# Kernel optimization log

Hardware: AMD Instinct MI355X
Metric: run time of the kernel (lower is better)

Reference implementation:

```python
import jax, jax.numpy as jnp
import numpy as np

B, L1, NUM_C, DIM_S, SIZE_M = 64, 199, 1000, 64, 50


def setup_inputs() -> dict:
    key = jax.random.key(0)
    ks = jax.random.split(key, 16)
    inp = {
        "cseqs": jax.random.randint(ks[0], (B, L1), 0, NUM_C),
        "rseqs": jax.random.randint(ks[1], (B, L1), 0, 2),
        "shft_cseqs": jax.random.randint(ks[2], (B, L1), 0, NUM_C),
        "shft_rseqs": jax.random.randint(ks[3], (B, L1), 0, 2),
        # learned parameters (linear weights stored as [in, out])
        "kemb": jax.random.normal(ks[4], (NUM_C, DIM_S)) * 0.05,
        "vemb": jax.random.normal(ks[5], (2 * NUM_C, DIM_S)) * 0.05,
        "Mk": jax.random.normal(ks[6], (SIZE_M, DIM_S)) * (2.0 / DIM_S) ** 0.5,
        "Mv0": jax.random.normal(ks[7], (SIZE_M, DIM_S)) * (2.0 / DIM_S) ** 0.5,
        "Wf": jax.random.normal(ks[8], (2 * DIM_S, DIM_S)) * 0.05,
        "bf": jnp.zeros((DIM_S,)),
        "We": jax.random.normal(ks[9], (DIM_S, DIM_S)) * 0.05,
        "be": jnp.zeros((DIM_S,)),
        "Wa": jax.random.normal(ks[10], (DIM_S, DIM_S)) * 0.05,
        "ba": jnp.zeros((DIM_S,)),
        "Wp": jax.random.normal(ks[11], (DIM_S, 1)) * 0.05,
        "bp": jnp.zeros((1,)),
    }
    return inp


def reference(cseqs, rseqs, shft_cseqs, shft_rseqs,
              kemb, vemb, Mk, Mv0, Wf, bf, We, be, Wa, ba, Wp, bp):
    # reconstruct full-length sequences: [B, L] with L = L1 + 1
    q = jnp.concatenate([cseqs[:, :1], shft_cseqs], axis=-1)
    r = jnp.concatenate([rseqs[:, :1], shft_rseqs], axis=-1)
    x = q + NUM_C * r

    k = kemb[q]                                  # [B, L, D]
    v = vemb[x]                                  # [B, L, D]

    w = jax.nn.softmax(k @ Mk.T, axis=-1)        # [B, L, M] correlation weights
    e = jax.nn.sigmoid(v @ We + be)              # [B, L, D] erase
    a = jnp.tanh(v @ Wa + ba)                    # [B, L, D] add

    def step(Mvt, inp):
        et, at, wt = inp                         # [B,D], [B,D], [B,M]
        Mv_prev = Mvt                            # memory BEFORE this update (used for read)
        Mvt = Mvt * (1.0 - wt[:, :, None] * et[:, None, :]) + wt[:, :, None] * at[:, None, :]
        return Mvt, Mv_prev

    Mv_init = jnp.broadcast_to(Mv0[None], (B, SIZE_M, DIM_S))
    _, Mv_prev = jax.lax.scan(
        step, Mv_init,
        (e.transpose(1, 0, 2), a.transpose(1, 0, 2), w.transpose(1, 0, 2)))
    Mv_prev = Mv_prev.transpose(1, 0, 2, 3)      # [B, L, M, D]

    read = jnp.einsum('blm,blmd->bld', w, Mv_prev)   # weighted read
    info = jnp.concatenate([read, k], axis=-1)       # [B, L, 2D]
    f = jnp.tanh(info @ Wf + bf)                     # dropout is identity in eval
    p = jax.nn.sigmoid((f @ Wp + bp).squeeze(-1))    # [B, L]
    return p
```

## Files before the change

### kernel.cpp

```cpp
#include <hip/hip_runtime.h>
#include <math.h>

#define B    64
#define L1   199
#define L    200
#define NC   1000
#define D    64
#define M    50
#define NCH  10
#define MC   5
#define TCC  50

__global__ __launch_bounds__(64) void phase0(
    const float* __restrict__ kemb, const float* __restrict__ vemb,
    const float* __restrict__ Mk,
    const float* __restrict__ We, const float* __restrict__ be,
    const float* __restrict__ Wa, const float* __restrict__ ba,
    const float* __restrict__ Wf,
    float* __restrict__ wtab, float* __restrict__ etab,
    float* __restrict__ atab, float* __restrict__ ktab)
{
    __shared__ __align__(16) float lrow[4 * D];
    const int lane = threadIdx.x;
    const int bid  = blockIdx.x;

    if (bid < 250) {
        const int r0 = bid * 4;
        #pragma unroll
        for (int i = 0; i < 4; ++i)
            lrow[i * D + lane] = kemb[(size_t)(r0 + i) * D + lane];
        __syncthreads();

        float Mk_r[D];
        {
            const int mrow = (lane < M) ? lane : (M - 1);
            #pragma unroll
            for (int d = 0; d < D; d += 4) {
                const float4 t4 = *(const float4*)(Mk + mrow * D + d);
                Mk_r[d] = t4.x; Mk_r[d+1] = t4.y; Mk_r[d+2] = t4.z; Mk_r[d+3] = t4.w;
            }
        }
        #pragma unroll
        for (int i = 0; i < 4; ++i) {
            float c0 = 0.f, c1 = 0.f;
            #pragma unroll
            for (int d = 0; d < D; d += 4) {
                const float4 kb = *(const float4*)&lrow[i * D + d];
                c0 = fmaf(Mk_r[d],     kb.x, c0);
                c1 = fmaf(Mk_r[d + 1], kb.y, c1);
                c0 = fmaf(Mk_r[d + 2], kb.z, c0);
                c1 = fmaf(Mk_r[d + 3], kb.w, c1);
            }
            const float logit = (lane < M) ? (c0 + c1) : -INFINITY;
            float mx = logit;
            #pragma unroll
            for (int off = 32; off; off >>= 1) mx = fmaxf(mx, __shfl_xor(mx, off, 64));
            const float ex = expf(logit - mx);
            float sm = ex;
            #pragma unroll
            for (int off = 32; off; off >>= 1) sm += __shfl_xor(sm, off, 64);
            if (lane < M) wtab[(size_t)(r0 + i) * M + lane] = ex / sm;
        }
    } else if (bid < 1250) {
        const bool is_e = (bid < 750);
        const int  r0   = (is_e ? (bid - 250) : (bid - 750)) * 4;
        #pragma unroll
        for (int i = 0; i < 4; ++i)
            lrow[i * D + lane] = vemb[(size_t)(r0 + i) * D + lane];
        __syncthreads();

        const float* __restrict__ W   = is_e ? We : Wa;
        float*       __restrict__ dst = is_e ? etab : atab;
        float Wc[D];
        #pragma unroll
        for (int din = 0; din < D; ++din) Wc[din] = W[din * D + lane];
        const float br = is_e ? be[lane] : ba[lane];

        #pragma unroll
        for (int i = 0; i < 4; ++i) {
            float c0 = 0.f, c1 = 0.f;
            #pragma unroll
            for (int d = 0; d < D; d += 4) {
                const float4 vb = *(const float4*)&lrow[i * D + d];
                c0 = fmaf(Wc[d],     vb.x, c0);
                c1 = fmaf(Wc[d + 1], vb.y, c1);
                c0 = fmaf(Wc[d + 2], vb.z, c0);
                c1 = fmaf(Wc[d + 3], vb.w, c1);
            }
            const float acc = c0 + c1;
            const float r = is_e ? (1.f / (1.f + expf(-(acc + br))))
                                 : tanhf(acc + br);
            dst[(size_t)(r0 + i) * D + lane] = r;
        }
    } else {
        const int r0 = (bid - 1250) * 4;
        #pragma unroll
        for (int i = 0; i < 4; ++i)
            lrow[i * D + lane] = kemb[(size_t)(r0 + i) * D + lane];
        __syncthreads();

        float Wc[D];
        #pragma unroll
        for (int i = 0; i < D; ++i) Wc[i] = Wf[(size_t)(D + i) * D + lane];

        #pragma unroll
        for (int i = 0; i < 4; ++i) {
            float f1 = 0.f;
            #pragma unroll
            for (int d = 0; d < D; d += 4) {
                const float4 kb = *(const float4*)&lrow[i * D + d];
                f1 = fmaf(Wc[d],     kb.x, f1);
                f1 = fmaf(Wc[d + 1], kb.y, f1);
                f1 = fmaf(Wc[d + 2], kb.z, f1);
                f1 = fmaf(Wc[d + 3], kb.w, f1);
            }
            ktab[(size_t)(r0 + i) * D + lane] = f1;
        }
    }
}

__global__ __launch_bounds__(64, 1) void phase2(
    const float* __restrict__ Mv0,
    const int* __restrict__ cseqs, const int* __restrict__ rseqs,
    const int* __restrict__ shft_cseqs, const int* __restrict__ shft_rseqs,
    const float* __restrict__ wtab, const float* __restrict__ etab,
    const float* __restrict__ atab, float* __restrict__ rp_out)
{
    __shared__ __align__(16) float lds_w[TCC * 8];
    const int lane = threadIdx.x;
    const int b  = blockIdx.x / NCH;
    const int ch = blockIdx.x % NCH;
    const int m0 = ch * MC;

    float Mv[MC];
    #pragma unroll
    for (int j = 0; j < MC; ++j) Mv[j] = Mv0[(m0 + j) * D + lane];

    float* __restrict__ rp = rp_out + ((size_t)b * L * NCH + ch) * D + lane;

    for (int tcb = 0; tcb < L / TCC; ++tcb) {
        const int t0 = tcb * TCC;

        int ql = 0, xl = 0;
        if (lane < TCC) {
            const int t = t0 + lane;
            int q, r;
            if (t == 0) { q = cseqs[b * L1];              r = rseqs[b * L1]; }
            else        { q = shft_cseqs[b * L1 + t - 1]; r = shft_rseqs[b * L1 + t - 1]; }
            ql = q; xl = q + NC * r;
        }
        if (lane < TCC) {
            const float* __restrict__ wp = wtab + (size_t)ql * M + m0;
            #pragma unroll
            for (int j = 0; j < MC; ++j) lds_w[lane * 8 + j] = wp[j];
        }
        float er[TCC], ar[TCC];
        #pragma unroll
        for (int t = 0; t < TCC; ++t) {
            const int s = __builtin_amdgcn_readlane(xl, t);
            er[t] = etab[(size_t)s * D + lane];
            ar[t] = atab[(size_t)s * D + lane];
        }
        __syncthreads();

        #pragma unroll
        for (int t = 0; t < TCC; ++t) {
            const float4 w4 = *(const float4*)&lds_w[t * 8];
            const float  wm0 = w4.x, wm1 = w4.y, wm2 = w4.z, wm3 = w4.w;
            const float  wm4 = lds_w[t * 8 + 4];
            const float ed = er[t], ad = ar[t];
            float r0 = 0.f, r1 = 0.f;
            r0 = fmaf(wm0, Mv[0], r0); Mv[0] = fmaf(Mv[0], -(wm0 * ed), fmaf(wm0, ad, Mv[0]));
            r1 = fmaf(wm1, Mv[1], r1); Mv[1] = fmaf(Mv[1], -(wm1 * ed), fmaf(wm1, ad, Mv[1]));
            r0 = fmaf(wm2, Mv[2], r0); Mv[2] = fmaf(Mv[2], -(wm2 * ed), fmaf(wm2, ad, Mv[2]));
            r1 = fmaf(wm3, Mv[3], r1); Mv[3] = fmaf(Mv[3], -(wm3 * ed), fmaf(wm3, ad, Mv[3]));
            r0 = fmaf(wm4, Mv[4], r0); Mv[4] = fmaf(Mv[4], -(wm4 * ed), fmaf(wm4, ad, Mv[4]));
            rp[(size_t)(t0 + t) * NCH * D] = r0 + r1;
        }
    }
}

__global__ __launch_bounds__(256, 1) void phase3(
    const int* __restrict__ cseqs, const int* __restrict__ shft_cseqs,
    const float* __restrict__ ktab,
    const float* __restrict__ Wf, const float* __restrict__ bf,
    const float* __restrict__ Wp, const float* __restrict__ bp,
    const float* __restrict__ rp, float* __restrict__ out)
{
    __shared__ __align__(16) float lds_rd[4 * D];
    const int tid  = threadIdx.x;
    const int lane = tid & 63;
    const int wave = tid >> 6;
    float* __restrict__ lrd = lds_rd + wave * D;

    float Wf_c[D];
    #pragma unroll
    for (int i = 0; i < D; ++i) Wf_c[i] = Wf[(size_t)i * D + lane];
    const float bf_r = bf[lane];
    const float wp_r = Wp[lane];
    const float bp_r = bp[0];

    const int base = blockIdx.x * 16 + wave * 4;

    int q4[4];
    #pragma unroll
    for (int p = 0; p < 4; ++p) {
        const int gpos = base + p;
        const int b = gpos / L, l = gpos % L;
        q4[p] = (l == 0) ? cseqs[b * L1] : shft_cseqs[b * L1 + l - 1];
    }

    #pragma unroll
    for (int p = 0; p < 4; ++p) {
        const int gpos = base + p;
        float rd = 0.f;
        #pragma unroll
        for (int ch = 0; ch < NCH; ++ch)
            rd += rp[((size_t)gpos * NCH + ch) * D + lane];
        const float kt = ktab[(size_t)q4[p] * D + lane];

        lrd[lane] = rd;
        float f0 = 0.f;
        #pragma unroll
        for (int i = 0; i < D; i += 4) {
            const float4 rb = *(const float4*)&lrd[i];
            f0 = fmaf(Wf_c[i],     rb.x, f0);
            f0 = fmaf(Wf_c[i + 1], rb.y, f0);
            f0 = fmaf(Wf_c[i + 2], rb.z, f0);
            f0 = fmaf(Wf_c[i + 3], rb.w, f0);
        }
        const float f = tanhf(f0 + kt + bf_r);

        float c = f * wp_r;
        #pragma unroll
        for (int off = 32; off; off >>= 1) c += __shfl_xor(c, off, 64);
        if (lane == 0) out[gpos] = 1.f / (1.f + expf(-(c + bp_r)));
    }
}

extern "C" void kernel_launch(void* const* d_in, const int* in_sizes, int n_in,
                              void* d_out, int out_size, void* d_ws, size_t ws_size,
                              hipStream_t stream) {
    const int*   cseqs      = (const int*)d_in[0];
    const int*   rseqs      = (const int*)d_in[1];
    const int*   shft_cseqs = (const int*)d_in[2];
    const int*   shft_rseqs = (const int*)d_in[3];
    const float* kemb = (const float*)d_in[4];
    const float* vemb = (const float*)d_in[5];
    const float* Mk   = (const float*)d_in[6];
    const float* Mv0  = (const float*)d_in[7];
    const float* Wf   = (const float*)d_in[8];
    const float* bf   = (const float*)d_in[9];
    const float* We   = (const float*)d_in[10];
    const float* be   = (const float*)d_in[11];
    const float* Wa   = (const float*)d_in[12];
    const float* ba   = (const float*)d_in[13];
    const float* Wp   = (const float*)d_in[14];
    const float* bp   = (const float*)d_in[15];
    float* out = (float*)d_out;

    float* ws   = (float*)d_ws;
    float* wtab = ws;
    float* etab = wtab + (size_t)NC * M;
    float* atab = etab + (size_t)2 * NC * D;
    float* ktab = atab + (size_t)2 * NC * D;
    float* rp   = ktab + (size_t)NC * D;

    phase0<<<dim3(1500), dim3(64), 0, stream>>>(
        kemb, vemb, Mk, We, be, Wa, ba, Wf, wtab, etab, atab, ktab);
    phase2<<<dim3(B * NCH), dim3(64), 0, stream>>>(
        Mv0, cseqs, rseqs, shft_cseqs, shft_rseqs, wtab, etab, atab, rp);
    phase3<<<dim3(800), dim3(256), 0, stream>>>(
        cseqs, shft_cseqs, ktab, Wf, bf, Wp, bp, rp, out);
}
```

Baseline: 127.8 us.

## Parallelize memory-update scan over time segments with affine prefix composition

Replaces the sequential 200-step recurrence per (batch, chunk) with a two-pass segmented scan. scanA computes, for each of the first three 50-step segments, the composed affine map (A, B) with Mv' = A*Mv + B. scanB then launches four segments in parallel, each rebuilding its starting memory from Mv0 and the preceding segment maps before running its own 50 steps and writing reads. This cuts the serial dependency chain and raises the block count fourfold, at the cost of an extra kernel launch, redundant gathers, and extra workspace traffic.

```diff
diff --git a/kernel.cpp b/kernel.cpp
--- a/kernel.cpp
+++ b/kernel.cpp
@@ -9,7 +9,8 @@
 #define M    50
 #define NCH  10
 #define MC   5
-#define TCC  50
+#define SEG  4
+#define TS   50
 
 __global__ __launch_bounds__(64) void phase0(
     const float* __restrict__ kemb, const float* __restrict__ vemb,
@@ -119,64 +120,130 @@
     }
 }
 
-__global__ __launch_bounds__(64, 1) void phase2(
+__global__ __launch_bounds__(64) void scanA(
+    const int* __restrict__ cseqs, const int* __restrict__ rseqs,
+    const int* __restrict__ shft_cseqs, const int* __restrict__ shft_rseqs,
+    const float* __restrict__ wtab, const float* __restrict__ etab,
+    const float* __restrict__ atab,
+    float* __restrict__ abuf, float* __restrict__ bbuf)
+{
+    __shared__ __align__(16) float lds_w[TS * 8];
+    const int lane = threadIdx.x;
+    const int s  = blockIdx.x % 3;
+    const int bc = blockIdx.x / 3;
+    const int b  = bc / NCH;
+    const int ch = bc % NCH;
+    const int m0 = ch * MC;
+    const int t0 = s * TS;
+
+    int ql = 0, xl = 0;
+    if (lane < TS) {
+        const int t = t0 + lane;
+        int q, r;
+        if (t == 0) { q = cseqs[b * L1];              r = rseqs[b * L1]; }
+        else        { q = shft_cseqs[b * L1 + t - 1]; r = shft_rseqs[b * L1 + t - 1]; }
+        ql = q; xl = q + NC * r;
+    }
+    if (lane < TS) {
+        const float* __restrict__ wp = wtab + (size_t)ql * M + m0;
+        #pragma unroll
+        for (int j = 0; j < MC; ++j) lds_w[lane * 8 + j] = wp[j];
+    }
+    float er[TS], ar[TS];
+    #pragma unroll
+    for (int t = 0; t < TS; ++t) {
+        const int sx = __builtin_amdgcn_readlane(xl, t);
+        er[t] = etab[(size_t)sx * D + lane];
+        ar[t] = atab[(size_t)sx * D + lane];
+    }
+    __syncthreads();
+
+    float A0=1.f,A1=1.f,A2=1.f,A3=1.f,A4=1.f;
+    float B0=0.f,B1=0.f,B2=0.f,B3=0.f,B4=0.f;
+
+    #pragma unroll
+    for (int t = 0; t < TS; ++t) {
+        const float4 w4 = *(const float4*)&lds_w[t * 8];
+        const float wm0 = w4.x, wm1 = w4.y, wm2 = w4.z, wm3 = w4.w;
+        const float wm4 = lds_w[t * 8 + 4];
+        const float ed = er[t], ad = ar[t];
+        A0 = fmaf(A0, -(wm0 * ed), A0); B0 = fmaf(B0, -(wm0 * ed), fmaf(wm0, ad, B0));
+        A1 = fmaf(A1, -(wm1 * ed), A1); B1 = fmaf(B1, -(wm1 * ed), fmaf(wm1, ad, B1));
+        A2 = fmaf(A2, -(wm2 * ed), A2); B2 = fmaf(B2, -(wm2 * ed), fmaf(wm2, ad, B2));
+        A3 = fmaf(A3, -(wm3 * ed), A3); B3 = fmaf(B3, -(wm3 * ed), fmaf(wm3, ad, B3));
+        A4 = fmaf(A4, -(wm4 * ed), A4); B4 = fmaf(B4, -(wm4 * ed), fmaf(wm4, ad, B4));
+    }
+    float* __restrict__ ap = abuf + ((size_t)bc * 3 + s) * MC * D + lane;
+    float* __restrict__ bp = bbuf + ((size_t)bc * 3 + s) * MC * D + lane;
+    ap[0 * D] = A0; ap[1 * D] = A1; ap[2 * D] = A2; ap[3 * D] = A3; ap[4 * D] = A4;
+    bp[0 * D] = B0; bp[1 * D] = B1; bp[2 * D] = B2; bp[3 * D] = B3; bp[4 * D] = B4;
+}
+
+__global__ __launch_bounds__(64) void scanB(
     const float* __restrict__ Mv0,
     const int* __restrict__ cseqs, const int* __restrict__ rseqs,
     const int* __restrict__ shft_cseqs, const int* __restrict__ shft_rseqs,
     const float* __restrict__ wtab, const float* __restrict__ etab,
-    const float* __restrict__ atab, float* __restrict__ rp_out)
+    const float* __restrict__ atab,
+    const float* __restrict__ abuf, const float* __restrict__ bbuf,
+    float* __restrict__ rp_out)
 {
-    __shared__ __align__(16) float lds_w[TCC * 8];
+    __shared__ __align__(16) float lds_w[TS * 8];
     const int lane = threadIdx.x;
-    const int b  = blockIdx.x / NCH;
-    const int ch = blockIdx.x % NCH;
+    const int s  = blockIdx.x % SEG;
+    const int bc = blockIdx.x / SEG;
+    const int b  = bc / NCH;
+    const int ch = bc % NCH;
     const int m0 = ch * MC;
+    const int t0 = s * TS;
+
+    int ql = 0, xl = 0;
+    if (lane < TS) {
+        const int t = t0 + lane;
+        int q, r;
+        if (t == 0) { q = cseqs[b * L1];              r = rseqs[b * L1]; }
+        else        { q = shft_cseqs[b * L1 + t - 1]; r = shft_rseqs[b * L1 + t - 1]; }
+        ql = q; xl = q + NC * r;
+    }
+    if (lane < TS) {
+        const float* __restrict__ wp = wtab + (size_t)ql * M + m0;
+        #pragma unroll
+        for (int j = 0; j < MC; ++j) lds_w[lane * 8 + j] = wp[j];
+    }
+    float er[TS], ar[TS];
+    #pragma unroll
+    for (int t = 0; t < TS; ++t) {
+        const int sx = __builtin_amdgcn_readlane(xl, t);
+        er[t] = etab[(size_t)sx * D + lane];
+        ar[t] = atab[(size_t)sx * D + lane];
+    }
 
     float Mv[MC];
     #pragma unroll
     for (int j = 0; j < MC; ++j) Mv[j] = Mv0[(m0 + j) * D + lane];
+    for (int ss = 0; ss < s; ++ss) {
+        const float* __restrict__ ap = abuf + ((size_t)bc * 3 + ss) * MC * D + lane;
+        const float* __restrict__ bp = bbuf + ((size_t)bc * 3 + ss) * MC * D + lane;
+        #pragma unroll
+        for (int j = 0; j < MC; ++j) Mv[j] = fmaf(ap[j * D], Mv[j], bp[j * D]);
+    }
+    __syncthreads();
 
     float* __restrict__ rp = rp_out + ((size_t)b * L * NCH + ch) * D + lane;
 
-    for (int tcb = 0; tcb < L / TCC; ++tcb) {
-        const int t0 = tcb * TCC;
-
-        int ql = 0, xl = 0;
-        if (lane < TCC) {
-            const int t = t0 + lane;
-            int q, r;
-            if (t == 0) { q = cseqs[b * L1];              r = rseqs[b * L1]; }
-            else        { q = shft_cseqs[b * L1 + t - 1]; r = shft_rseqs[b * L1 + t - 1]; }
-            ql = q; xl = q + NC * r;
-        }
-        if (lane < TCC) {
-            const float* __restrict__ wp = wtab + (size_t)ql * M + m0;
-            #pragma unroll
-            for (int j = 0; j < MC; ++j) lds_w[lane * 8 + j] = wp[j];
-        }
-        float er[TCC], ar[TCC];
-        #pragma unroll
-        for (int t = 0; t < TCC; ++t) {
-            const int s = __builtin_amdgcn_readlane(xl, t);
-            er[t] = etab[(size_t)s * D + lane];
-            ar[t] = atab[(size_t)s * D + lane];
-        }
-        __syncthreads();
-
-        #pragma unroll
-        for (int t = 0; t < TCC; ++t) {
-            const float4 w4 = *(const float4*)&lds_w[t * 8];
-            const float  wm0 = w4.x, wm1 = w4.y, wm2 = w4.z, wm3 = w4.w;
-            const float  wm4 = lds_w[t * 8 + 4];
-            const float ed = er[t], ad = ar[t];
-            float r0 = 0.f, r1 = 0.f;
-            r0 = fmaf(wm0, Mv[0], r0); Mv[0] = fmaf(Mv[0], -(wm0 * ed), fmaf(wm0, ad, Mv[0]));
-            r1 = fmaf(wm1, Mv[1], r1); Mv[1] = fmaf(Mv[1], -(wm1 * ed), fmaf(wm1, ad, Mv[1]));
-            r0 = fmaf(wm2, Mv[2], r0); Mv[2] = fmaf(Mv[2], -(wm2 * ed), fmaf(wm2, ad, Mv[2]));
-            r1 = fmaf(wm3, Mv[3], r1); Mv[3] = fmaf(Mv[3], -(wm3 * ed), fmaf(wm3, ad, Mv[3]));
-            r0 = fmaf(wm4, Mv[4], r0); Mv[4] = fmaf(Mv[4], -(wm4 * ed), fmaf(wm4, ad, Mv[4]));
-            rp[(size_t)(t0 + t) * NCH * D] = r0 + r1;
-        }
+    #pragma unroll
+    for (int t = 0; t < TS; ++t) {
+        const float4 w4 = *(const float4*)&lds_w[t * 8];
+        const float wm0 = w4.x, wm1 = w4.y, wm2 = w4.z, wm3 = w4.w;
+        const float wm4 = lds_w[t * 8 + 4];
+        const float ed = er[t], ad = ar[t];
+        float r0 = 0.f, r1 = 0.f;
+        r0 = fmaf(wm0, Mv[0], r0); Mv[0] = fmaf(Mv[0], -(wm0 * ed), fmaf(wm0, ad, Mv[0]));
+        r1 = fmaf(wm1, Mv[1], r1); Mv[1] = fmaf(Mv[1], -(wm1 * ed), fmaf(wm1, ad, Mv[1]));
+        r0 = fmaf(wm2, Mv[2], r0); Mv[2] = fmaf(Mv[2], -(wm2 * ed), fmaf(wm2, ad, Mv[2]));
+        r1 = fmaf(wm3, Mv[3], r1); Mv[3] = fmaf(Mv[3], -(wm3 * ed), fmaf(wm3, ad, Mv[3]));
+        r0 = fmaf(wm4, Mv[4], r0); Mv[4] = fmaf(Mv[4], -(wm4 * ed), fmaf(wm4, ad, Mv[4]));
+        rp[(size_t)(t0 + t) * NCH * D] = r0 + r1;
     }
 }
 
@@ -265,11 +332,16 @@
     float* atab = etab + (size_t)2 * NC * D;
     float* ktab = atab + (size_t)2 * NC * D;
     float* rp   = ktab + (size_t)NC * D;
+    float* abuf = rp   + (size_t)B * L * NCH * D;
+    float* bbuf = abuf + (size_t)B * NCH * 3 * MC * D;
 
     phase0<<<dim3(1500), dim3(64), 0, stream>>>(
         kemb, vemb, Mk, We, be, Wa, ba, Wf, wtab, etab, atab, ktab);
-    phase2<<<dim3(B * NCH), dim3(64), 0, stream>>>(
-        Mv0, cseqs, rseqs, shft_cseqs, shft_rseqs, wtab, etab, atab, rp);
+    scanA<<<dim3(B * NCH * 3), dim3(64), 0, stream>>>(
+        cseqs, rseqs, shft_cseqs, shft_rseqs, wtab, etab, atab, abuf, bbuf);
+    scanB<<<dim3(B * NCH * SEG), dim3(64), 0, stream>>>(
+        Mv0, cseqs, rseqs, shft_cseqs, shft_rseqs, wtab, etab, atab,
+        abuf, bbuf, rp);
     phase3<<<dim3(800), dim3(256), 0, stream>>>(
         cseqs, shft_cseqs, ktab, Wf, bf, Wp, bp, rp, out);
 }
```

New measurement: 127.4 us. No clear change (-0.3%).

## Fuse phases into cooperative kernel with time-segmented affine scan

Applied to the files above, without the earlier changes.

Replaces the three launches with one cooperative kernel that uses grid syncs. The recurrence is split into four time segments per batch. Each of the first three segments computes the affine composition (A, B) of its updates. Later segments then combine the earlier compositions to get their starting memory state, so the serial scan runs over 50 steps instead of 200. Partial reads are reduced in LDS and the output MLP is fused in, which removes the rp round trip through global memory. The cost is extra redundant arithmetic, two grid-wide barriers, and 256 blocks of 320 threads that must all be co-resident.

```diff
diff --git a/kernel.cpp b/kernel.cpp
--- a/kernel.cpp
+++ b/kernel.cpp
@@ -1,5 +1,8 @@
 #include <hip/hip_runtime.h>
+#include <hip/hip_cooperative_groups.h>
 #include <math.h>
+
+namespace cg = cooperative_groups;
 
 #define B    64
 #define L1   199
@@ -7,234 +10,251 @@
 #define NC   1000
 #define D    64
 #define M    50
-#define NCH  10
-#define MC   5
-#define TCC  50
-
-__global__ __launch_bounds__(64) void phase0(
+#define SEG  4
+#define TS   50
+#define WV   5
+#define MPW  10
+#define BLK  320
+#define GRID 256
+
+__global__ __launch_bounds__(BLK, 1) void fused(
+    const int* __restrict__ cseqs, const int* __restrict__ rseqs,
+    const int* __restrict__ shft_cseqs, const int* __restrict__ shft_rseqs,
     const float* __restrict__ kemb, const float* __restrict__ vemb,
-    const float* __restrict__ Mk,
+    const float* __restrict__ Mk, const float* __restrict__ Mv0,
     const float* __restrict__ We, const float* __restrict__ be,
     const float* __restrict__ Wa, const float* __restrict__ ba,
-    const float* __restrict__ Wf,
-    float* __restrict__ wtab, float* __restrict__ etab,
-    float* __restrict__ atab, float* __restrict__ ktab)
-{
-    __shared__ __align__(16) float lrow[4 * D];
-    const int lane = threadIdx.x;
-    const int bid  = blockIdx.x;
-
-    if (bid < 250) {
-        const int r0 = bid * 4;
-        #pragma unroll
-        for (int i = 0; i < 4; ++i)
-            lrow[i * D + lane] = kemb[(size_t)(r0 + i) * D + lane];
-        __syncthreads();
-
-        float Mk_r[D];
-        {
-            const int mrow = (lane < M) ? lane : (M - 1);
-            #pragma unroll
-            for (int d = 0; d < D; d += 4) {
-                const float4 t4 = *(const float4*)(Mk + mrow * D + d);
-                Mk_r[d] = t4.x; Mk_r[d+1] = t4.y; Mk_r[d+2] = t4.z; Mk_r[d+3] = t4.w;
-            }
-        }
-        #pragma unroll
-        for (int i = 0; i < 4; ++i) {
-            float c0 = 0.f, c1 = 0.f;
-            #pragma unroll
-            for (int d = 0; d < D; d += 4) {
-                const float4 kb = *(const float4*)&lrow[i * D + d];
-                c0 = fmaf(Mk_r[d],     kb.x, c0);
-                c1 = fmaf(Mk_r[d + 1], kb.y, c1);
-                c0 = fmaf(Mk_r[d + 2], kb.z, c0);
-                c1 = fmaf(Mk_r[d + 3], kb.w, c1);
-            }
-            const float logit = (lane < M) ? (c0 + c1) : -INFINITY;
-            float mx = logit;
-            #pragma unroll
-            for (int off = 32; off; off >>= 1) mx = fmaxf(mx, __shfl_xor(mx, off, 64));
-            const float ex = expf(logit - mx);
-            float sm = ex;
-            #pragma unroll
-            for (int off = 32; off; off >>= 1) sm += __shfl_xor(sm, off, 64);
-            if (lane < M) wtab[(size_t)(r0 + i) * M + lane] = ex / sm;
-        }
-    } else if (bid < 1250) {
-        const bool is_e = (bid < 750);
-        const int  r0   = (is_e ? (bid - 250) : (bid - 750)) * 4;
-        #pragma unroll
-        for (int i = 0; i < 4; ++i)
-            lrow[i * D + lane] = vemb[(size_t)(r0 + i) * D + lane];
-        __syncthreads();
-
-        const float* __restrict__ W   = is_e ? We : Wa;
-        float*       __restrict__ dst = is_e ? etab : atab;
-        float Wc[D];
-        #pragma unroll
-        for (int din = 0; din < D; ++din) Wc[din] = W[din * D + lane];
-        const float br = is_e ? be[lane] : ba[lane];
-
-        #pragma unroll
-        for (int i = 0; i < 4; ++i) {
-            float c0 = 0.f, c1 = 0.f;
-            #pragma unroll
-            for (int d = 0; d < D; d += 4) {
-                const float4 vb = *(const float4*)&lrow[i * D + d];
-                c0 = fmaf(Wc[d],     vb.x, c0);
-                c1 = fmaf(Wc[d + 1], vb.y, c1);
-                c0 = fmaf(Wc[d + 2], vb.z, c0);
-                c1 = fmaf(Wc[d + 3], vb.w, c1);
-            }
-            const float acc = c0 + c1;
-            const float r = is_e ? (1.f / (1.f + expf(-(acc + br))))
-                                 : tanhf(acc + br);
-            dst[(size_t)(r0 + i) * D + lane] = r;
-        }
-    } else {
-        const int r0 = (bid - 1250) * 4;
-        #pragma unroll
-        for (int i = 0; i < 4; ++i)
-            lrow[i * D + lane] = kemb[(size_t)(r0 + i) * D + lane];
-        __syncthreads();
-
-        float Wc[D];
-        #pragma unroll
-        for (int i = 0; i < D; ++i) Wc[i] = Wf[(size_t)(D + i) * D + lane];
-
-        #pragma unroll
-        for (int i = 0; i < 4; ++i) {
-            float f1 = 0.f;
-            #pragma unroll
-            for (int d = 0; d < D; d += 4) {
-                const float4 kb = *(const float4*)&lrow[i * D + d];
-                f1 = fmaf(Wc[d],     kb.x, f1);
-                f1 = fmaf(Wc[d + 1], kb.y, f1);
-                f1 = fmaf(Wc[d + 2], kb.z, f1);
-                f1 = fmaf(Wc[d + 3], kb.w, f1);
-            }
-            ktab[(size_t)(r0 + i) * D + lane] = f1;
-        }
-    }
-}
-
-__global__ __launch_bounds__(64, 1) void phase2(
-    const float* __restrict__ Mv0,
-    const int* __restrict__ cseqs, const int* __restrict__ rseqs,
-    const int* __restrict__ shft_cseqs, const int* __restrict__ shft_rseqs,
-    const float* __restrict__ wtab, const float* __restrict__ etab,
-    const float* __restrict__ atab, float* __restrict__ rp_out)
-{
-    __shared__ __align__(16) float lds_w[TCC * 8];
-    const int lane = threadIdx.x;
-    const int b  = blockIdx.x / NCH;
-    const int ch = blockIdx.x % NCH;
-    const int m0 = ch * MC;
-
-    float Mv[MC];
-    #pragma unroll
-    for (int j = 0; j < MC; ++j) Mv[j] = Mv0[(m0 + j) * D + lane];
-
-    float* __restrict__ rp = rp_out + ((size_t)b * L * NCH + ch) * D + lane;
-
-    for (int tcb = 0; tcb < L / TCC; ++tcb) {
-        const int t0 = tcb * TCC;
-
-        int ql = 0, xl = 0;
-        if (lane < TCC) {
-            const int t = t0 + lane;
-            int q, r;
-            if (t == 0) { q = cseqs[b * L1];              r = rseqs[b * L1]; }
-            else        { q = shft_cseqs[b * L1 + t - 1]; r = shft_rseqs[b * L1 + t - 1]; }
-            ql = q; xl = q + NC * r;
-        }
-        if (lane < TCC) {
-            const float* __restrict__ wp = wtab + (size_t)ql * M + m0;
-            #pragma unroll
-            for (int j = 0; j < MC; ++j) lds_w[lane * 8 + j] = wp[j];
-        }
-        float er[TCC], ar[TCC];
-        #pragma unroll
-        for (int t = 0; t < TCC; ++t) {
-            const int s = __builtin_amdgcn_readlane(xl, t);
-            er[t] = etab[(size_t)s * D + lane];
-            ar[t] = atab[(size_t)s * D + lane];
-        }
-        __syncthreads();
-
-        #pragma unroll
-        for (int t = 0; t < TCC; ++t) {
-            const float4 w4 = *(const float4*)&lds_w[t * 8];
-            const float  wm0 = w4.x, wm1 = w4.y, wm2 = w4.z, wm3 = w4.w;
-            const float  wm4 = lds_w[t * 8 + 4];
-            const float ed = er[t], ad = ar[t];
-            float r0 = 0.f, r1 = 0.f;
-            r0 = fmaf(wm0, Mv[0], r0); Mv[0] = fmaf(Mv[0], -(wm0 * ed), fmaf(wm0, ad, Mv[0]));
-            r1 = fmaf(wm1, Mv[1], r1); Mv[1] = fmaf(Mv[1], -(wm1 * ed), fmaf(wm1, ad, Mv[1]));
-            r0 = fmaf(wm2, Mv[2], r0); Mv[2] = fmaf(Mv[2], -(wm2 * ed), fmaf(wm2, ad, Mv[2]));
-            r1 = fmaf(wm3, Mv[3], r1); Mv[3] = fmaf(Mv[3], -(wm3 * ed), fmaf(wm3, ad, Mv[3]));
-            r0 = fmaf(wm4, Mv[4], r0); Mv[4] = fmaf(Mv[4], -(wm4 * ed), fmaf(wm4, ad, Mv[4]));
-            rp[(size_t)(t0 + t) * NCH * D] = r0 + r1;
-        }
-    }
-}
-
-__global__ __launch_bounds__(256, 1) void phase3(
-    const int* __restrict__ cseqs, const int* __restrict__ shft_cseqs,
-    const float* __restrict__ ktab,
     const float* __restrict__ Wf, const float* __restrict__ bf,
     const float* __restrict__ Wp, const float* __restrict__ bp,
-    const float* __restrict__ rp, float* __restrict__ out)
+    float* __restrict__ out,
+    float* __restrict__ wtab, float* __restrict__ etab,
+    float* __restrict__ atab, float* __restrict__ ktab,
+    float* __restrict__ abuf, float* __restrict__ bbuf)
 {
-    __shared__ __align__(16) float lds_rd[4 * D];
+    __shared__ __align__(16) float s_part[WV][TS][D];
+    __shared__ __align__(16) float s_ea[2][TS][D];
+    __shared__ __align__(16) float s_w[TS][M];
+    __shared__ int s_q[TS];
+    __shared__ int s_x[TS];
+
     const int tid  = threadIdx.x;
     const int lane = tid & 63;
-    const int wave = tid >> 6;
-    float* __restrict__ lrd = lds_rd + wave * D;
-
-    float Wf_c[D];
+    const int wv   = tid >> 6;
+    const int blk  = blockIdx.x;
+    cg::grid_group grid = cg::this_grid();
+
+    {
+        float* lrow = &s_part[wv][0][0];
+        for (int task = blk * WV + wv; task < 1500; task += GRID * WV) {
+            if (task < 250) {
+                const int r0 = task * 4;
+                #pragma unroll
+                for (int i = 0; i < 4; ++i)
+                    lrow[i * D + lane] = kemb[(size_t)(r0 + i) * D + lane];
+                float Mk_r[D];
+                {
+                    const int mrow = (lane < M) ? lane : (M - 1);
+                    #pragma unroll
+                    for (int d = 0; d < D; d += 4) {
+                        const float4 t4 = *(const float4*)(Mk + mrow * D + d);
+                        Mk_r[d]=t4.x; Mk_r[d+1]=t4.y; Mk_r[d+2]=t4.z; Mk_r[d+3]=t4.w;
+                    }
+                }
+                #pragma unroll
+                for (int i = 0; i < 4; ++i) {
+                    float c0 = 0.f, c1 = 0.f;
+                    #pragma unroll
+                    for (int d = 0; d < D; d += 4) {
+                        const float4 kb = *(const float4*)&lrow[i * D + d];
+                        c0 = fmaf(Mk_r[d],     kb.x, c0);
+                        c1 = fmaf(Mk_r[d + 1], kb.y, c1);
+                        c0 = fmaf(Mk_r[d + 2], kb.z, c0);
+                        c1 = fmaf(Mk_r[d + 3], kb.w, c1);
+                    }
+                    const float logit = (lane < M) ? (c0 + c1) : -INFINITY;
+                    float mx = logit;
+                    #pragma unroll
+                    for (int off = 32; off; off >>= 1) mx = fmaxf(mx, __shfl_xor(mx, off, 64));
+                    const float ex = expf(logit - mx);
+                    float sm = ex;
+                    #pragma unroll
+                    for (int off = 32; off; off >>= 1) sm += __shfl_xor(sm, off, 64);
+                    if (lane < M) wtab[(size_t)(r0 + i) * M + lane] = ex / sm;
+                }
+            } else if (task < 1250) {
+                const bool is_e = (task < 750);
+                const int  r0   = (is_e ? (task - 250) : (task - 750)) * 4;
+                #pragma unroll
+                for (int i = 0; i < 4; ++i)
+                    lrow[i * D + lane] = vemb[(size_t)(r0 + i) * D + lane];
+                const float* __restrict__ W   = is_e ? We : Wa;
+                float*       __restrict__ dst = is_e ? etab : atab;
+                float Wc[D];
+                #pragma unroll
+                for (int din = 0; din < D; ++din) Wc[din] = W[din * D + lane];
+                const float br = is_e ? be[lane] : ba[lane];
+                #pragma unroll
+                for (int i = 0; i < 4; ++i) {
+                    float c0 = 0.f, c1 = 0.f;
+                    #pragma unroll
+                    for (int d = 0; d < D; d += 4) {
+                        const float4 vb = *(const float4*)&lrow[i * D + d];
+                        c0 = fmaf(Wc[d],     vb.x, c0);
+                        c1 = fmaf(Wc[d + 1], vb.y, c1);
+                        c0 = fmaf(Wc[d + 2], vb.z, c0);
+                        c1 = fmaf(Wc[d + 3], vb.w, c1);
+                    }
+                    const float acc = c0 + c1;
+                    const float r = is_e ? (1.f / (1.f + expf(-(acc + br))))
+                                         : tanhf(acc + br);
+                    dst[(size_t)(r0 + i) * D + lane] = r;
+                }
+            } else {
+                const int r0 = (task - 1250) * 4;
+                #pragma unroll
+                for (int i = 0; i < 4; ++i)
+                    lrow[i * D + lane] = kemb[(size_t)(r0 + i) * D + lane];
+                float Wc[D];
+                #pragma unroll
+                for (int i = 0; i < D; ++i) Wc[i] = Wf[(size_t)(D + i) * D + lane];
+                #pragma unroll
+                for (int i = 0; i < 4; ++i) {
+                    float f1 = 0.f;
+                    #pragma unroll
+                    for (int d = 0; d < D; d += 4) {
+                        const float4 kb = *(const float4*)&lrow[i * D + d];
+                        f1 = fmaf(Wc[d],     kb.x, f1);
+                        f1 = fmaf(Wc[d + 1], kb.y, f1);
+                        f1 = fmaf(Wc[d + 2], kb.z, f1);
+                        f1 = fmaf(Wc[d + 3], kb.w, f1);
+                    }
+                    ktab[(size_t)(r0 + i) * D + lane] = f1;
+                }
+            }
+        }
+    }
+    grid.sync();
+
+    const int b  = blk >> 2;
+    const int s  = blk & 3;
+    const int t0 = s * TS;
+    const int m0 = wv * MPW;
+
+    if (wv == 0 && lane < TS) {
+        const int t = t0 + lane;
+        int q, r;
+        if (t == 0) { q = cseqs[b * L1];              r = rseqs[b * L1]; }
+        else        { q = shft_cseqs[b * L1 + t - 1]; r = shft_rseqs[b * L1 + t - 1]; }
+        s_q[lane] = q;
+        s_x[lane] = q + NC * r;
+    }
+    __syncthreads();
+
     #pragma unroll
-    for (int i = 0; i < D; ++i) Wf_c[i] = Wf[(size_t)i * D + lane];
-    const float bf_r = bf[lane];
-    const float wp_r = Wp[lane];
-    const float bp_r = bp[0];
-
-    const int base = blockIdx.x * 16 + wave * 4;
-
-    int q4[4];
+    for (int j = 0; j < MPW; ++j) {
+        const int t = wv * MPW + j;
+        const int x = s_x[t];
+        s_ea[0][t][lane] = etab[(size_t)x * D + lane];
+        s_ea[1][t][lane] = atab[(size_t)x * D + lane];
+    }
+    if (lane < TS) {
+        const int qq = s_q[lane];
+        const float* __restrict__ wp_ = wtab + (size_t)qq * M + m0;
+        #pragma unroll
+        for (int j = 0; j < MPW; ++j) s_w[lane][m0 + j] = wp_[j];
+    }
+    __syncthreads();
+
+    if (s < 3) {
+        float A[MPW], Bv[MPW];
+        #pragma unroll
+        for (int j = 0; j < MPW; ++j) { A[j] = 1.f; Bv[j] = 0.f; }
+        for (int t = 0; t < TS; ++t) {
+            const float ed = s_ea[0][t][lane];
+            const float ad = s_ea[1][t][lane];
+            #pragma unroll
+            for (int j = 0; j < MPW; ++j) {
+                const float wm = s_w[t][m0 + j];
+                const float we = wm * ed;
+                A[j]  = fmaf(A[j],  -we, A[j]);
+                Bv[j] = fmaf(Bv[j], -we, fmaf(wm, ad, Bv[j]));
+            }
+        }
+        #pragma unroll
+        for (int j = 0; j < MPW; ++j) {
+            abuf[((size_t)(b * 3 + s) * M + m0 + j) * D + lane] = A[j];
+            bbuf[((size_t)(b * 3 + s) * M + m0 + j) * D + lane] = Bv[j];
+        }
+    }
+    grid.sync();
+
+    float Mv[MPW];
     #pragma unroll
-    for (int p = 0; p < 4; ++p) {
-        const int gpos = base + p;
-        const int b = gpos / L, l = gpos % L;
-        q4[p] = (l == 0) ? cseqs[b * L1] : shft_cseqs[b * L1 + l - 1];
-    }
-
-    #pragma unroll
-    for (int p = 0; p < 4; ++p) {
-        const int gpos = base + p;
-        float rd = 0.f;
-        #pragma unroll
-        for (int ch = 0; ch < NCH; ++ch)
-            rd += rp[((size_t)gpos * NCH + ch) * D + lane];
-        const float kt = ktab[(size_t)q4[p] * D + lane];
-
-        lrd[lane] = rd;
-        float f0 = 0.f;
-        #pragma unroll
-        for (int i = 0; i < D; i += 4) {
-            const float4 rb = *(const float4*)&lrd[i];
-            f0 = fmaf(Wf_c[i],     rb.x, f0);
-            f0 = fmaf(Wf_c[i + 1], rb.y, f0);
-            f0 = fmaf(Wf_c[i + 2], rb.z, f0);
-            f0 = fmaf(Wf_c[i + 3], rb.w, f0);
-        }
-        const float f = tanhf(f0 + kt + bf_r);
-
-        float c = f * wp_r;
-        #pragma unroll
-        for (int off = 32; off; off >>= 1) c += __shfl_xor(c, off, 64);
-        if (lane == 0) out[gpos] = 1.f / (1.f + expf(-(c + bp_r)));
+    for (int j = 0; j < MPW; ++j) Mv[j] = Mv0[(m0 + j) * D + lane];
+    for (int ss = 0; ss < s; ++ss) {
+        #pragma unroll
+        for (int j = 0; j < MPW; ++j) {
+            const float a_ = abuf[((size_t)(b * 3 + ss) * M + m0 + j) * D + lane];
+            const float b_ = bbuf[((size_t)(b * 3 + ss) * M + m0 + j) * D + lane];
+            Mv[j] = fmaf(a_, Mv[j], b_);
+        }
+    }
+
+    for (int t = 0; t < TS; ++t) {
+        const float ed = s_ea[0][t][lane];
+        const float ad = s_ea[1][t][lane];
+        float r0a = 0.f, r1a = 0.f, r0b = 0.f, r1b = 0.f;
+        #pragma unroll
+        for (int j = 0; j < 5; ++j) {
+            const float wm = s_w[t][m0 + j];
+            if (j & 1) r1a = fmaf(wm, Mv[j], r1a);
+            else       r0a = fmaf(wm, Mv[j], r0a);
+            const float we = wm * ed;
+            Mv[j] = fmaf(Mv[j], -we, fmaf(wm, ad, Mv[j]));
+        }
+        #pragma unroll
+        for (int j = 5; j < 10; ++j) {
+            const float wm = s_w[t][m0 + j];
+            if ((j - 5) & 1) r1b = fmaf(wm, Mv[j], r1b);
+            else             r0b = fmaf(wm, Mv[j], r0b);
+            const float we = wm * ed;
+            Mv[j] = fmaf(Mv[j], -we, fmaf(wm, ad, Mv[j]));
+        }
+        s_part[wv][t][lane] = (r0a + r1a) + (r0b + r1b);
+    }
+    __syncthreads();
+
+    {
+        float Wf_c[D];
+        #pragma unroll
+        for (int i = 0; i < D; ++i) Wf_c[i] = Wf[(size_t)i * D + lane];
+        const float bf_r = bf[lane];
+        const float wp_r = Wp[lane];
+        const float bp_r = bp[0];
+
+        #pragma unroll
+        for (int j = 0; j < MPW; ++j) {
+            const int t = wv * MPW + j;
+            const float rd = (((s_part[0][t][lane] + s_part[1][t][lane])
+                              + s_part[2][t][lane]) + s_part[3][t][lane])
+                              + s_part[4][t][lane];
+            const float kt = ktab[(size_t)s_q[t] * D + lane];
+            s_ea[0][t][lane] = rd;
+            float f0 = 0.f;
+            #pragma unroll
+            for (int i = 0; i < D; i += 4) {
+                const float4 rb = *(const float4*)&s_ea[0][t][i];
+                f0 = fmaf(Wf_c[i],     rb.x, f0);
+                f0 = fmaf(Wf_c[i + 1], rb.y, f0);
+                f0 = fmaf(Wf_c[i + 2], rb.z, f0);
+                f0 = fmaf(Wf_c[i + 3], rb.w, f0);
+            }
+            const float f = tanhf(f0 + kt + bf_r);
+            float c = f * wp_r;
+            #pragma unroll
+            for (int off = 32; off; off >>= 1) c += __shfl_xor(c, off, 64);
+            if (lane == 0) out[b * L + t0 + t] = 1.f / (1.f + expf(-(c + bp_r)));
+        }
     }
 }
 
@@ -264,12 +284,16 @@
     float* etab = wtab + (size_t)NC * M;
     float* atab = etab + (size_t)2 * NC * D;
     float* ktab = atab + (size_t)2 * NC * D;
-    float* rp   = ktab + (size_t)NC * D;
-
-    phase0<<<dim3(1500), dim3(64), 0, stream>>>(
-        kemb, vemb, Mk, We, be, Wa, ba, Wf, wtab, etab, atab, ktab);
-    phase2<<<dim3(B * NCH), dim3(64), 0, stream>>>(
-        Mv0, cseqs, rseqs, shft_cseqs, shft_rseqs, wtab, etab, atab, rp);
-    phase3<<<dim3(800), dim3(256), 0, stream>>>(
-        cseqs, shft_cseqs, ktab, Wf, bf, Wp, bp, rp, out);
+    float* abuf = ktab + (size_t)NC * D;
+    float* bbuf = abuf + (size_t)B * 3 * M * D;
+
+    void* args[] = {
+        (void*)&cseqs, (void*)&rseqs, (void*)&shft_cseqs, (void*)&shft_rseqs,
+        (void*)&kemb, (void*)&vemb, (void*)&Mk, (void*)&Mv0,
+        (void*)&We, (void*)&be, (void*)&Wa, (void*)&ba,
+        (void*)&Wf, (void*)&bf, (void*)&Wp, (void*)&bp,
+        (void*)&out, (void*)&wtab, (void*)&etab, (void*)&atab,
+        (void*)&ktab, (void*)&abuf, (void*)&bbuf };
+
+    hipLaunchCooperativeKernel((void*)fused, dim3(GRID), dim3(BLK), args, 0, stream);
 }
```

Measured after the change: 196.6 us. +53.8%, slower.
